# Performance work log

Measured on AMD Instinct MI355X. Metric: run time of the kernel, lower is better.

Reference implementation:

```python
import jax, jax.numpy as jnp
import numpy as np

N, D, E, K = 8192, 1024, 16, 2
CAP = 1024  # capacity_per_expert


def setup_inputs() -> dict:
    key = jax.random.key(0)
    k1, k2, k3 = jax.random.split(key, 3)
    return {
        "moe_inp": jax.random.normal(k1, (N, D), dtype=jnp.float32),
        "gate_w": jax.random.normal(k2, (D, E), dtype=jnp.float32) * 0.02,
        "gate_b": jnp.zeros((E,), dtype=jnp.float32),
        "expert_w": jax.random.normal(k3, (E, D, D), dtype=jnp.float32) * 0.02,
        "expert_b": jnp.zeros((E, D), dtype=jnp.float32),
    }


def _capacity_keep_mask(expert_id, slot_score, num_experts, capacity):
    """For each flattened (token, k) slot assigned to an expert, keep only the
    `capacity` slots with the highest token score (gate_score.max over k),
    matching the argsort-based drop in _fmoe_limited_global_forward."""
    nslots = expert_id.shape[0]
    # sort slots by (expert asc, score desc)
    order = jnp.lexsort((-slot_score, expert_id))
    counts = jnp.bincount(expert_id, length=num_experts)
    starts = jnp.concatenate([jnp.zeros((1,), counts.dtype), jnp.cumsum(counts)[:-1]])
    pos_in_expert = jnp.arange(nslots) - starts[expert_id[order]]
    keep_sorted = pos_in_expert < capacity
    return jnp.zeros((nslots,), dtype=bool).at[order].set(keep_sorted)


def reference(moe_inp, gate_w, gate_b, expert_w, expert_b):
    n, d = moe_inp.shape
    e = expert_w.shape[0]
    # NaiveGate: linear -> top-k -> softmax over the k selected logits
    logits = moe_inp @ gate_w + gate_b                       # [N, E]
    top_v, top_i = jax.lax.top_k(logits, K)                  # [N, K]
    gate_score = jax.nn.softmax(top_v, axis=-1)              # [N, K]

    expert_id = top_i.reshape(-1)                            # [N*K]
    token_id = jnp.arange(n * K) // K                        # [N*K]
    mask_scores = gate_score.max(axis=-1)                    # [N] per-token score
    slot_score = mask_scores[token_id]                       # [N*K]

    keep = _capacity_keep_mask(expert_id, slot_score, e, CAP).reshape(n, K)

    # expert forward: FMoELinear y = x @ W_e^T + b_e (dense over experts, then gather)
    all_out = jnp.einsum('nd,efd->nef', moe_inp, expert_w) + expert_b  # [N, E, D]
    y = jnp.take_along_axis(all_out, top_i[:, :, None], axis=1)        # [N, K, D]
    # dropped (over-capacity) slots pass the scattered input through unchanged
    y = jnp.where(keep[:, :, None], y, moe_inp[:, None, :])
    # combine: bmm(gate_score [N,1,K], y [N,K,D]) -> [N, D]
    return jnp.einsum('nk,nkd->nd', gate_score, y)
```

## Files before the change

### kernel.cpp

```cpp
#include <hip/hip_runtime.h>
#include <hip/hip_bf16.h>
#include <math.h>

#define N_TOK 8192
#define DIM   1024
#define NEXP  16
#define TOPK  2
#define CAPE  1024
#define NSLOT (N_TOK*TOPK)

typedef __attribute__((ext_vector_type(8))) short     short8;
typedef __attribute__((ext_vector_type(4))) float     floatx4;
typedef __attribute__((ext_vector_type(4))) unsigned short ushort4v;

__device__ __forceinline__ unsigned short f2bf(float f) {
    unsigned u = __float_as_uint(f);
    u += 0x7FFFu + ((u >> 16) & 1u);
    return (unsigned short)(u >> 16);
}

#define GLOAD_LDS16(g, l) __builtin_amdgcn_global_load_lds( \
    (const __attribute__((address_space(1))) unsigned int*)(g), \
    (__attribute__((address_space(3))) unsigned int*)(l), 16, 0, 0)

#define RAW_BARRIER() asm volatile("s_barrier" ::: "memory")

__global__ void cvt_gwt_zero_kernel(const float* __restrict__ ew,
                                    unsigned short* __restrict__ Wb,
                                    const float* __restrict__ gw,
                                    float* __restrict__ gwT,
                                    int* __restrict__ zws) {
    const int i = blockIdx.x * 256 + threadIdx.x;
    if (blockIdx.x == 0 && threadIdx.x < 64) zws[threadIdx.x] = 0;
    if (i < DIM * NEXP) {
        int d = i >> 4, e = i & 15;
        gwT[e * DIM + d] = gw[i];
    }
    floatx4 v = ((const floatx4*)ew)[i];
    ushort4v o;
    o[0] = f2bf(v[0]); o[1] = f2bf(v[1]); o[2] = f2bf(v[2]); o[3] = f2bf(v[3]);
    ((ushort4v*)Wb)[i] = o;
}

__global__ __launch_bounds__(256) void gate_kernel(
        const float* __restrict__ x,
        const float* __restrict__ gwT,
        const float* __restrict__ gb,
        int* __restrict__ slot_expert,
        unsigned long long* __restrict__ slot_key,
        float* __restrict__ slot_gate,
        unsigned short* __restrict__ Xb,
        int* __restrict__ counts,
        unsigned long long* __restrict__ buckets,
        int* __restrict__ slot_bpos) {
    __shared__ int se[8];
    __shared__ unsigned long long sk[8];
    __shared__ int lcnt[NEXP], lbase[NEXP], lpo[8];
    const int tid  = threadIdx.x;
    const int wv   = tid >> 6;
    const int t    = blockIdx.x * 4 + wv;
    const int lane = tid & 63;
    if (tid < NEXP) lcnt[tid] = 0;

    const floatx4* xr = (const floatx4*)(x + (size_t)t * DIM);
    ushort4v* Xb4 = (ushort4v*)Xb + (size_t)t * 256;
    floatx4 xv[4];
#pragma unroll
    for (int i = 0; i < 4; i++) {
        xv[i] = xr[lane + i * 64];
        ushort4v o;
        o[0] = f2bf(xv[i][0]); o[1] = f2bf(xv[i][1]);
        o[2] = f2bf(xv[i][2]); o[3] = f2bf(xv[i][3]);
        Xb4[lane + i * 64] = o;
    }

    float acc[NEXP];
#pragma unroll
    for (int e = 0; e < NEXP; e++) {
        const floatx4* wr = (const floatx4*)(gwT + (size_t)e * DIM);
        float a = 0.f;
#pragma unroll
        for (int i = 0; i < 4; i++) {
            floatx4 w = wr[lane + i * 64];
            a += xv[i][0]*w[0] + xv[i][1]*w[1] + xv[i][2]*w[2] + xv[i][3]*w[3];
        }
        acc[e] = a;
    }
#pragma unroll
    for (int off = 32; off > 0; off >>= 1) {
#pragma unroll
        for (int e = 0; e < NEXP; e++) acc[e] += __shfl_down(acc[e], off, 64);
    }
    if (lane == 0) {
        float v0 = -1e30f; int i0 = 0;
#pragma unroll
        for (int e = 0; e < NEXP; e++) {
            float v = acc[e] + gb[e];
            acc[e] = v;
            if (v > v0) { v0 = v; i0 = e; }
        }
        float v1 = -1e30f; int i1 = 0;
#pragma unroll
        for (int e = 0; e < NEXP; e++) {
            if (e != i0 && acc[e] > v1) { v1 = acc[e]; i1 = e; }
        }
        float e1 = expf(v1 - v0);
        float den = 1.f + e1;
        float g0 = 1.f / den;
        float g1 = e1 / den;
        unsigned sb = __float_as_uint(g0);
        int s0 = 2 * t, s1 = 2 * t + 1;
        slot_expert[s0] = i0; slot_expert[s1] = i1;
        slot_gate[s0]   = g0; slot_gate[s1]   = g1;
        unsigned long long hi = ((unsigned long long)sb) << 32;
        unsigned long long k0 = hi | (unsigned)(0xFFFFFFFFu - (unsigned)s0);
        unsigned long long k1 = hi | (unsigned)(0xFFFFFFFFu - (unsigned)s1);
        slot_key[s0] = k0; slot_key[s1] = k1;
        se[2 * wv] = i0; se[2 * wv + 1] = i1;
        sk[2 * wv] = k0; sk[2 * wv + 1] = k1;
    }
    __syncthreads();
    if (tid < 8) lpo[tid] = atomicAdd(&lcnt[se[tid]], 1);
    __syncthreads();
    if (tid < NEXP) lbase[tid] = lcnt[tid] ? atomicAdd(&counts[tid], lcnt[tid]) : 0;
    __syncthreads();
    if (tid < 8) {
        int e = se[tid];
        int p = lbase[e] + lpo[tid];
        buckets[(size_t)e * NSLOT + p] = sk[tid];
        slot_bpos[blockIdx.x * 8 + tid] = p;
    }
}

__global__ __launch_bounds__(256) void keep_compact_kernel(
        const int* __restrict__ slot_expert,
        const unsigned long long* __restrict__ slot_key,
        const int* __restrict__ counts,
        const unsigned long long* __restrict__ buckets,
        int* __restrict__ slot_keep,
        int* __restrict__ elist,
        int* __restrict__ slot_pos) {
    const int wv   = threadIdx.x >> 6;
    const int lane = threadIdx.x & 63;
    const int s    = blockIdx.x * 4 + wv;
    const int e    = slot_expert[s];
    const int c    = counts[e];
    int kp = 1, pos;
    if (c <= CAPE) {
        pos = slot_keep[s];
    } else {
        const unsigned long long k = slot_key[s];
        const unsigned long long* bk = buckets + (size_t)e * NSLOT;
        int rank = 0;
        for (int i = lane; i < c; i += 64) rank += (bk[i] > k) ? 1 : 0;
#pragma unroll
        for (int off = 32; off > 0; off >>= 1) rank += __shfl_down(rank, off, 64);
        rank = __shfl(rank, 0, 64);
        kp  = (rank < CAPE) ? 1 : 0;
        pos = rank;
    }
    if (lane == 0) {
        slot_keep[s] = kp;
        if (kp) {
            int p = e * CAPE + pos;
            elist[p]    = s;
            slot_pos[s] = p;
        }
    }
}

__global__ void base_kernel(const float* __restrict__ x,
                            const int* __restrict__ keep,
                            const float* __restrict__ gate,
                            float* __restrict__ out) {
    int i = blockIdx.x * blockDim.x + threadIdx.x;
    int t = i >> 8;
    float c = 0.f;
    if (!keep[2 * t])     c += gate[2 * t];
    if (!keep[2 * t + 1]) c += gate[2 * t + 1];
    floatx4 v = ((const floatx4*)x)[i];
    ((floatx4*)out)[i] = v * c;
}

template <bool STORE_YS>
__global__ __launch_bounds__(512, 4)
void moe_gemm(const unsigned short* __restrict__ Xb,
              const unsigned short* __restrict__ Wb,
              const float* __restrict__ eb,
              const int* __restrict__ elist,
              const int* __restrict__ counts,
              const float* __restrict__ slot_gate,
              float* __restrict__ ys,
              float* __restrict__ out) {
    __shared__ unsigned short As[2][256 * 32];
    __shared__ unsigned short Bs[2][128 * 32];

    const int e  = blockIdx.z;
    int ne = counts[e]; if (ne > CAPE) ne = CAPE;
    const int m0 = blockIdx.y * 256;
    if (m0 >= ne) return;
    const int n0   = blockIdx.x * 128;
    const int tid  = threadIdx.x;
    const int wv   = tid >> 6;
    const int lane = tid & 63;
    const int q    = lane >> 4;
    const int l15  = lane & 15;
    const int wm   = (wv >> 1) * 64;
    const int wn   = (wv & 1) * 64;

    const int srow = wv * 16 + (lane >> 2);
    const int jsrc = (lane & 3) ^ ((lane >> 3) & 3);
    const unsigned short* gA0;
    const unsigned short* gA1;
    {
        int m = m0 + srow;
        int slot = elist[e * CAPE + (m < ne ? m : 0)];
        gA0 = Xb + (size_t)(slot >> 1) * DIM + jsrc * 8;
        m = m0 + 128 + srow;
        slot = elist[e * CAPE + (m < ne ? m : 0)];
        gA1 = Xb + (size_t)(slot >> 1) * DIM + jsrc * 8;
    }
    const unsigned short* gB0 =
        Wb + (size_t)e * DIM * DIM + (size_t)(n0 + srow) * DIM + jsrc * 8;

#define STAGE(b, k0) do { \
    GLOAD_LDS16(gA0 + (k0), &As[b][(wv * 16) * 32]); \
    GLOAD_LDS16(gA1 + (k0), &As[b][(128 + wv * 16) * 32]); \
    GLOAD_LDS16(gB0 + (k0), &Bs[b][(wv * 16) * 32]); } while (0)

    STAGE(0, 0);
    STAGE(1, 32);

    const int swz  = (q ^ ((l15 >> 1) & 3)) * 8;
    const int aoff = (wm + l15) * 32 + swz;
    const int boff = (wn + l15) * 32 + swz;

    floatx4 acc[4][4] = {};
    short8 a[4], b[4];

    for (int t = 0; t < 32; t++) {
        const int cur = t & 1;
        if (t == 31) { asm volatile("s_waitcnt vmcnt(0)" ::: "memory"); }
        else         { asm volatile("s_waitcnt vmcnt(3)" ::: "memory"); }
        __builtin_amdgcn_sched_barrier(0);
        RAW_BARRIER();

        const unsigned short* A_ = &As[cur][0];
        const unsigned short* B_ = &Bs[cur][0];
#pragma unroll
        for (int fi = 0; fi < 4; fi++) a[fi] = *(const short8*)(A_ + aoff + fi * 512);
#pragma unroll
        for (int fj = 0; fj < 4; fj++) b[fj] = *(const short8*)(B_ + boff + fj * 512);

        __builtin_amdgcn_s_setprio(1);
#pragma unroll
        for (int fi = 0; fi < 4; fi++)
#pragma unroll
            for (int fj = 0; fj < 4; fj++)
                acc[fi][fj] = __builtin_amdgcn_mfma_f32_16x16x32_bf16(
                    a[fi], b[fj], acc[fi][fj], 0, 0, 0);
        __builtin_amdgcn_s_setprio(0);
        RAW_BARRIER();

        if (t + 2 < 32) STAGE(cur, (t + 2) * 32);
    }
#undef STAGE

    float ebv[4];
#pragma unroll
    for (int fj = 0; fj < 4; fj++)
        ebv[fj] = eb[e * DIM + n0 + wn + fj * 16 + l15];
#pragma unroll
    for (int fi = 0; fi < 4; fi++) {
        const int mrow = m0 + wm + fi * 16 + q * 4;
#pragma unroll
        for (int r = 0; r < 4; r++) {
            int m = mrow + r;
            if (m >= ne) continue;
            if (STORE_YS) {
                float* yrow = ys + ((size_t)e * CAPE + m) * DIM + n0 + wn;
#pragma unroll
                for (int fj = 0; fj < 4; fj++)
                    yrow[fj * 16 + l15] = acc[fi][fj][r] + ebv[fj];
            } else {
                int slot = elist[e * CAPE + m];
                int tok  = slot >> 1;
                float g  = slot_gate[slot];
                float* orow = out + (size_t)tok * DIM + n0 + wn;
#pragma unroll
                for (int fj = 0; fj < 4; fj++)
                    atomicAdd(orow + fj * 16 + l15, g * (acc[fi][fj][r] + ebv[fj]));
            }
        }
    }
}

__global__ void combine_kernel(const float* __restrict__ x,
                               const float* __restrict__ ys,
                               const int* __restrict__ keep,
                               const int* __restrict__ pos,
                               const float* __restrict__ gate,
                               float* __restrict__ out) {
    int i = blockIdx.x * 256 + threadIdx.x;
    int t = i >> 8;
    int c = i & 255;
    int s0 = 2 * t, s1 = s0 + 1;
    int k0 = keep[s0], k1 = keep[s1];
    float g0 = gate[s0], g1 = gate[s1];
    floatx4 xv = {};
    if (!k0 || !k1) xv = ((const floatx4*)x)[i];
    floatx4 r;
    if (k0) {
        floatx4 y0 = ((const floatx4*)ys)[((size_t)pos[s0] << 8) + c];
        r = y0 * g0;
    } else r = xv * g0;
    if (k1) {
        floatx4 y1 = ((const floatx4*)ys)[((size_t)pos[s1] << 8) + c];
        r += y1 * g1;
    } else r += xv * g1;
    ((floatx4*)out)[i] = r;
}

extern "C" void kernel_launch(void* const* d_in, const int* in_sizes, int n_in,
                              void* d_out, int out_size, void* d_ws, size_t ws_size,
                              hipStream_t stream) {
    const float* x  = (const float*)d_in[0];
    const float* gw = (const float*)d_in[1];
    const float* gb = (const float*)d_in[2];
    const float* ew = (const float*)d_in[3];
    const float* eb = (const float*)d_in[4];
    float* out = (float*)d_out;

    char* ws = (char*)d_ws;
    int* counts      = (int*)(ws + 0);
    int* slot_expert = (int*)(ws + 256);
    int* slot_keep   = (int*)(ws + 65792);
    float* slot_gate = (float*)(ws + 131328);
    unsigned long long* slot_key = (unsigned long long*)(ws + 196864);
    unsigned long long* buckets  = (unsigned long long*)(ws + 327936);
    int* elist       = (int*)(ws + 2425088);
    float* gwT       = (float*)(ws + 2490624);
    unsigned short* Xb = (unsigned short*)(ws + 2556160);
    unsigned short* Wb = (unsigned short*)(ws + 19333376);
    int* slot_pos    = (int*)(ws + 52887808);
    float* ys        = (float*)(ws + 52953344);
    const size_t WS_NEED_YS = 52953344ull + (size_t)NEXP * CAPE * DIM * 4;

    const bool ys_path = (ws_size >= WS_NEED_YS);

    cvt_gwt_zero_kernel<<<(NEXP * DIM * DIM / 4) / 256, 256, 0, stream>>>(
        ew, Wb, gw, gwT, (int*)ws);
    gate_kernel<<<N_TOK / 4, 256, 0, stream>>>(x, gwT, gb, slot_expert, slot_key,
                                               slot_gate, Xb, counts, buckets,
                                               slot_keep);
    keep_compact_kernel<<<NSLOT / 4, 256, 0, stream>>>(slot_expert, slot_key, counts,
                                                       buckets, slot_keep, elist,
                                                       slot_pos);

    if (ys_path) {
        moe_gemm<true><<<dim3(8, 4, 16), 512, 0, stream>>>(Xb, Wb, eb, elist, counts,
                                                           slot_gate, ys, out);
        combine_kernel<<<N_TOK, 256, 0, stream>>>(x, ys, slot_keep, slot_pos,
                                                  slot_gate, out);
    } else {
        base_kernel<<<(N_TOK * DIM / 4) / 256, 256, 0, stream>>>(x, slot_keep,
                                                                 slot_gate, out);
        moe_gemm<false><<<dim3(8, 4, 16), 512, 0, stream>>>(Xb, Wb, eb, elist, counts,
                                                            slot_gate, nullptr, out);
    }
}
```

Measured before the change: 246.0 us.

## Restructure gate kernel to stage 16 tokens in LDS per block

The gate kernel now processes 16 tokens per block instead of 4. It stages each token's fp32 row in swizzled shared memory, then has each thread compute one (token, expert) logit serially, with no cross-lane shuffle reduction. This removes the 16-way shuffle reduction per token and reuses gate-weight loads across tokens in a block. In exchange it uses 64KB of LDS per block, which limits occupancy, and each thread runs a 256-iteration serial loop.

```diff
diff --git a/kernel.cpp b/kernel.cpp
--- a/kernel.cpp
+++ b/kernel.cpp
@@ -53,56 +53,60 @@
         int* __restrict__ counts,
         unsigned long long* __restrict__ buckets,
         int* __restrict__ slot_bpos) {
-    __shared__ int se[8];
-    __shared__ unsigned long long sk[8];
-    __shared__ int lcnt[NEXP], lbase[NEXP], lpo[8];
-    const int tid  = threadIdx.x;
-    const int wv   = tid >> 6;
-    const int t    = blockIdx.x * 4 + wv;
-    const int lane = tid & 63;
+    __shared__ float xs[16][1024];
+    __shared__ float lg[16][17];
+    __shared__ int se[32];
+    __shared__ unsigned long long sk[32];
+    __shared__ int lcnt[NEXP], lbase[NEXP], lpo[32];
+    const int tid = threadIdx.x;
+    const int t0  = blockIdx.x * 16;
     if (tid < NEXP) lcnt[tid] = 0;
 
-    const floatx4* xr = (const floatx4*)(x + (size_t)t * DIM);
-    ushort4v* Xb4 = (ushort4v*)Xb + (size_t)t * 256;
-    floatx4 xv[4];
-#pragma unroll
-    for (int i = 0; i < 4; i++) {
-        xv[i] = xr[lane + i * 64];
+    const floatx4* xg = (const floatx4*)(x + (size_t)t0 * DIM);
+    ushort4v* xb4 = (ushort4v*)Xb + (size_t)t0 * 256;
+#pragma unroll 4
+    for (int j = 0; j < 16; j++) {
+        int idx = tid + j * 256;
+        int tt = idx >> 8, c = idx & 255;
+        floatx4 v = xg[idx];
         ushort4v o;
-        o[0] = f2bf(xv[i][0]); o[1] = f2bf(xv[i][1]);
-        o[2] = f2bf(xv[i][2]); o[3] = f2bf(xv[i][3]);
-        Xb4[lane + i * 64] = o;
-    }
-
-    float acc[NEXP];
-#pragma unroll
-    for (int e = 0; e < NEXP; e++) {
+        o[0] = f2bf(v[0]); o[1] = f2bf(v[1]); o[2] = f2bf(v[2]); o[3] = f2bf(v[3]);
+        xb4[idx] = o;
+        *(floatx4*)&xs[tt][(c ^ (tt & 3)) * 4] = v;
+    }
+    __syncthreads();
+
+    {
+        const int tl = tid >> 4, e = tid & 15;
         const floatx4* wr = (const floatx4*)(gwT + (size_t)e * DIM);
-        float a = 0.f;
-#pragma unroll
-        for (int i = 0; i < 4; i++) {
-            floatx4 w = wr[lane + i * 64];
-            a += xv[i][0]*w[0] + xv[i][1]*w[1] + xv[i][2]*w[2] + xv[i][3]*w[3];
-        }
-        acc[e] = a;
-    }
-#pragma unroll
-    for (int off = 32; off > 0; off >>= 1) {
-#pragma unroll
-        for (int e = 0; e < NEXP; e++) acc[e] += __shfl_down(acc[e], off, 64);
-    }
-    if (lane == 0) {
+        const int tswz = tl & 3;
+        floatx4 acc = {0.f, 0.f, 0.f, 0.f};
+#pragma unroll 8
+        for (int c = 0; c < 256; c++) {
+            floatx4 xv = *(const floatx4*)&xs[tl][(c ^ tswz) * 4];
+            floatx4 wv = wr[c];
+            acc[0] += xv[0] * wv[0];
+            acc[1] += xv[1] * wv[1];
+            acc[2] += xv[2] * wv[2];
+            acc[3] += xv[3] * wv[3];
+        }
+        lg[tl][e] = (acc[0] + acc[1]) + (acc[2] + acc[3]) + gb[e];
+    }
+    __syncthreads();
+
+    if (tid < 16) {
+        const int t = t0 + tid;
         float v0 = -1e30f; int i0 = 0;
 #pragma unroll
         for (int e = 0; e < NEXP; e++) {
-            float v = acc[e] + gb[e];
-            acc[e] = v;
+            float v = lg[tid][e];
             if (v > v0) { v0 = v; i0 = e; }
         }
         float v1 = -1e30f; int i1 = 0;
 #pragma unroll
         for (int e = 0; e < NEXP; e++) {
-            if (e != i0 && acc[e] > v1) { v1 = acc[e]; i1 = e; }
+            float v = lg[tid][e];
+            if (e != i0 && v > v1) { v1 = v; i1 = e; }
         }
         float e1 = expf(v1 - v0);
         float den = 1.f + e1;
@@ -116,19 +120,19 @@
         unsigned long long k0 = hi | (unsigned)(0xFFFFFFFFu - (unsigned)s0);
         unsigned long long k1 = hi | (unsigned)(0xFFFFFFFFu - (unsigned)s1);
         slot_key[s0] = k0; slot_key[s1] = k1;
-        se[2 * wv] = i0; se[2 * wv + 1] = i1;
-        sk[2 * wv] = k0; sk[2 * wv + 1] = k1;
-    }
-    __syncthreads();
-    if (tid < 8) lpo[tid] = atomicAdd(&lcnt[se[tid]], 1);
+        se[2 * tid] = i0; se[2 * tid + 1] = i1;
+        sk[2 * tid] = k0; sk[2 * tid + 1] = k1;
+    }
+    __syncthreads();
+    if (tid < 32) lpo[tid] = atomicAdd(&lcnt[se[tid]], 1);
     __syncthreads();
     if (tid < NEXP) lbase[tid] = lcnt[tid] ? atomicAdd(&counts[tid], lcnt[tid]) : 0;
     __syncthreads();
-    if (tid < 8) {
+    if (tid < 32) {
         int e = se[tid];
         int p = lbase[e] + lpo[tid];
         buckets[(size_t)e * NSLOT + p] = sk[tid];
-        slot_bpos[blockIdx.x * 8 + tid] = p;
+        slot_bpos[blockIdx.x * 32 + tid] = p;
     }
 }
 
@@ -350,9 +354,9 @@
 
     cvt_gwt_zero_kernel<<<(NEXP * DIM * DIM / 4) / 256, 256, 0, stream>>>(
         ew, Wb, gw, gwT, (int*)ws);
-    gate_kernel<<<N_TOK / 4, 256, 0, stream>>>(x, gwT, gb, slot_expert, slot_key,
-                                               slot_gate, Xb, counts, buckets,
-                                               slot_keep);
+    gate_kernel<<<N_TOK / 16, 256, 0, stream>>>(x, gwT, gb, slot_expert, slot_key,
+                                                slot_gate, Xb, counts, buckets,
+                                                slot_keep);
     keep_compact_kernel<<<NSLOT / 4, 256, 0, stream>>>(slot_expert, slot_key, counts,
                                                        buckets, slot_keep, elist,
                                                        slot_pos);
```

After: 274.1 us. +11.4%, slower.
